# Performance work log

Measured on AMD Instinct MI355X. Metric: run time of the kernel, lower is better.

## Reference

```python
import jax, jax.numpy as jnp
import numpy as np

NEG_SLOPE = 0.2  # leaky_relu negative slope (alpha)

def _glorot(key, shape):
    fan_in, fan_out = shape[0], shape[-1]
    lim = jnp.sqrt(6.0 / (fan_in + fan_out))
    return jax.random.uniform(key, shape, jnp.float32, -lim, lim)

def setup_inputs() -> dict:
    key = jax.random.key(0)
    ks = jax.random.split(key, 10)
    N, E, F_IN, HID, HEADS, NCLASS = 50000, 800000, 512, 32, 8, 32
    x = jax.random.normal(ks[0], (N, F_IN), jnp.float32)
    edge_index = jax.random.randint(ks[1], (2, E), 0, N, jnp.int64)
    # layer 1: heads=8, out per head = 32, concat -> 256
    W1 = _glorot(ks[2], (F_IN, HEADS * HID))
    att_src1 = _glorot(ks[3], (HEADS, HID))
    att_dst1 = _glorot(ks[4], (HEADS, HID))
    b1 = jnp.zeros((HEADS * HID,), jnp.float32)
    # layer 2: heads=1, out = nclass
    W2 = _glorot(ks[5], (HEADS * HID, NCLASS))
    att_src2 = _glorot(ks[6], (1, NCLASS))
    att_dst2 = _glorot(ks[7], (1, NCLASS))
    b2 = jnp.zeros((NCLASS,), jnp.float32)
    return {"x": x, "edge_index": edge_index, "W1": W1, "att_src1": att_src1,
            "att_dst1": att_dst1, "b1": b1, "W2": W2, "att_src2": att_src2,
            "att_dst2": att_dst2, "b2": b2}

def gat_conv(x, src, dst, W, a_src, a_dst, bias, num_nodes):
    """PyG GATConv (eval mode, self loops already appended to src/dst)."""
    H, C = a_src.shape
    h = (x @ W).reshape(num_nodes, H, C)                 # [N,H,C]
    score_src = jnp.einsum('nhc,hc->nh', h, a_src)       # [N,H]
    score_dst = jnp.einsum('nhc,hc->nh', h, a_dst)       # [N,H]
    e = jax.nn.leaky_relu(score_src[src] + score_dst[dst], NEG_SLOPE)  # [E,H]
    m = jax.ops.segment_max(e, dst, num_segments=num_nodes)           # [N,H]
    w = jnp.exp(e - m[dst])
    denom = jax.ops.segment_sum(w, dst, num_segments=num_nodes)       # [N,H]
    alpha = w / (denom[dst] + 1e-16)                                  # [E,H]
    out = jax.ops.segment_sum(alpha[:, :, None] * h[src], dst,
                              num_segments=num_nodes)                 # [N,H,C]
    return out.reshape(num_nodes, H * C) + bias

def reference(x, edge_index, W1, att_src1, att_dst1, b1, W2, att_src2, att_dst2, b2):
    N = x.shape[0]
    loops = jnp.arange(N, dtype=edge_index.dtype)
    src = jnp.concatenate([edge_index[0], loops])  # PyG add_self_loops=True
    dst = jnp.concatenate([edge_index[1], loops])
    h = jax.nn.elu(gat_conv(x, src, dst, W1, att_src1, att_dst1, b1, N))
    out = gat_conv(h, src, dst, W2, att_src2, att_dst2, b2, N)
    return out + 1e-06
```

## Files before the change

kernel.cpp:

```cpp
#include <hip/hip_runtime.h>
#include <math.h>

#define N_NODES 50000
#define N_EDGES 800000
#define E2 (N_EDGES + N_NODES)
#define F_IN 512
#define HEADS 8
#define HID 32
#define HC 256
#define NCLASS 32
#define NEG_SLOPE 0.2f
#define ELLW 64

typedef unsigned int uint;
typedef unsigned short ushort;
typedef __attribute__((ext_vector_type(8))) short bf16x8;
typedef __attribute__((ext_vector_type(4))) float f32x4;

#define GLOBAL_LOAD_LDS16(g, l) \
    __builtin_amdgcn_global_load_lds((const __attribute__((address_space(1))) void*)(g), \
                                     (__attribute__((address_space(3))) void*)(l), 16, 0, 0)

__device__ inline uint bf16_rne_bits(float f) {
    uint u = __float_as_uint(f);
    return (u + 0x7fffu + ((u >> 16) & 1u)) >> 16;
}
__device__ inline float bf2f(ushort u) { return __uint_as_float(((uint)u) << 16); }

#define W1_BLOCKS 512
#define W2_BLOCKS 32
#define FILL_BLOCKS ((E2 / 4 + 255) / 256)

__global__ void __launch_bounds__(256) prep_kernel(const float* __restrict__ W1,
        ushort* __restrict__ w1hi, ushort* __restrict__ w1lo,
        const float* __restrict__ W2, ushort* __restrict__ w2hi, ushort* __restrict__ w2lo,
        const int* __restrict__ ei, int* __restrict__ cursor, int* __restrict__ ell) {
    int b = blockIdx.x;
    if (b < W1_BLOCKS) {
        int t = b * 256 + threadIdx.x;
        int n = t >> 9, k = t & 511;
        float f = W1[k * 256 + n];
        uint h = bf16_rne_bits(f);
        float r = f - __uint_as_float(h << 16);
        w1hi[t] = (ushort)h;
        w1lo[t] = (ushort)bf16_rne_bits(r);
    } else if (b < W1_BLOCKS + W2_BLOCKS) {
        int t = (b - W1_BLOCKS) * 256 + threadIdx.x;
        int n = t >> 8, k = t & 255;
        float f = W2[k * 32 + n];
        uint h = bf16_rne_bits(f);
        float r = f - __uint_as_float(h << 16);
        w2hi[t] = (ushort)h;
        w2lo[t] = (ushort)bf16_rne_bits(r);
    } else {
        int e0 = ((b - W1_BLOCKS - W2_BLOCKS) * 256 + threadIdx.x) * 4;
        if (e0 < E2) {
            int src[4], dst[4];
            if (e0 < N_EDGES) {
                int4 s4 = *(const int4*)(ei + e0);
                int4 d4 = *(const int4*)(ei + N_EDGES + e0);
                src[0] = s4.x; src[1] = s4.y; src[2] = s4.z; src[3] = s4.w;
                dst[0] = d4.x; dst[1] = d4.y; dst[2] = d4.z; dst[3] = d4.w;
            } else {
                #pragma unroll
                for (int j = 0; j < 4; ++j) { src[j] = e0 + j - N_EDGES; dst[j] = src[j]; }
            }
            #pragma unroll
            for (int j = 0; j < 4; ++j) {
                int d = dst[j];
                int p = atomicAdd(&cursor[d], 1);
                ell[d * ELLW + p] = src[j];
            }
        }
    }
}

__global__ void __launch_bounds__(256) gemm1_mfma_kernel(const uint* __restrict__ xp,
        const ushort* __restrict__ bhi, const ushort* __restrict__ blo,
        const float* __restrict__ as1, const float* __restrict__ ad1,
        ushort* __restrict__ C, float* __restrict__ ssrc, float* __restrict__ sdst, int M) {
    __shared__ uint   As[2][128 * 32];
    __shared__ ushort Bh[2][128 * 32];
    __shared__ ushort Bl[2][128 * 32];
    const int tid = threadIdx.x, lane = tid & 63, wave = tid >> 6;

    const int NW = ((N_NODES + 127) / 128) * 2;
    const int orig = blockIdx.y * gridDim.x + blockIdx.x;
    const int xcd = orig & 7, idx = orig >> 3;
    const int q = NW >> 3, r = NW & 7;
    const int nid = (xcd < r ? xcd * (q + 1) : r * (q + 1) + (xcd - r) * q) + idx;
    const int bm = (nid >> 1) * 128, bn = (nid & 1) * 128;

    const uint* agp[8]; const uint* alp[8];
    #pragma unroll
    for (int s = 0; s < 4; ++s) {
        int t = wave * 4 + s;
        int p = t * 64 + lane;
        int row = p >> 3, cs = p & 7;
        int c = cs ^ (row & 7);
        int grow = bm + row; if (grow > M - 1) grow = M - 1;
        agp[s]     = xp + ((size_t)grow * 512 + c * 4);
        agp[s + 4] = xp + ((size_t)grow * 512 + 32 + c * 4);
        alp[s]     = &As[0][t * 256];
        alp[s + 4] = &As[1][t * 256];
    }
    const ushort* bhgp[4]; const ushort* blgp[4]; const ushort* bhlp[4]; const ushort* bllp[4];
    #pragma unroll
    for (int s = 0; s < 2; ++s) {
        int t = wave * 2 + s;
        int p = t * 64 + lane;
        int row = p >> 2, qs = p & 3;
        int qq = qs ^ ((row >> 1) & 3);
        size_t go0 = (size_t)(bn + row) * 512 + qq * 8;
        size_t go1 = go0 + 32;
        bhgp[s] = bhi + go0; bhgp[s + 2] = bhi + go1;
        blgp[s] = blo + go0; blgp[s + 2] = blo + go1;
        bhlp[s] = &Bh[0][t * 512]; bhlp[s + 2] = &Bh[1][t * 512];
        bllp[s] = &Bl[0][t * 512]; bllp[s + 2] = &Bl[1][t * 512];
    }

    f32x4 acc[4][4] = {};
    const int wm = (wave >> 1) * 64, wn = (wave & 1) * 64;
    const int fm = lane & 15, quad = lane >> 4;

    for (int kk = 0; kk < 8; ++kk) {
        #pragma unroll
        for (int s = 0; s < 8; ++s) GLOBAL_LOAD_LDS16(agp[s], alp[s]);
        #pragma unroll
        for (int s = 0; s < 4; ++s) {
            GLOBAL_LOAD_LDS16(bhgp[s], bhlp[s]);
            GLOBAL_LOAD_LDS16(blgp[s], bllp[s]);
        }
        #pragma unroll
        for (int s = 0; s < 8; ++s) agp[s] += 64;
        #pragma unroll
        for (int s = 0; s < 4; ++s) { bhgp[s] += 64; blgp[s] += 64; }
        __syncthreads();

        #pragma unroll
        for (int h = 0; h < 2; ++h) {
            bf16x8 ah[4], al[4], bh[4], bl[4];
            #pragma unroll
            for (int i = 0; i < 4; ++i) {
                int row = wm + i * 16 + fm;
                int sw = row & 7;
                uint4 c0 = *(const uint4*)&As[h][row * 32 + (((2 * quad)     ^ sw) * 4)];
                uint4 c1 = *(const uint4*)&As[h][row * 32 + (((2 * quad + 1) ^ sw) * 4)];
                union { uint u[4]; bf16x8 v; } H, L;
                H.u[0] = __builtin_amdgcn_perm(c0.y, c0.x, 0x07060302u);
                H.u[1] = __builtin_amdgcn_perm(c0.w, c0.z, 0x07060302u);
                H.u[2] = __builtin_amdgcn_perm(c1.y, c1.x, 0x07060302u);
                H.u[3] = __builtin_amdgcn_perm(c1.w, c1.z, 0x07060302u);
                uint r0 = __float_as_uint(__uint_as_float(c0.x) - __uint_as_float(c0.x & 0xffff0000u));
                uint r1 = __float_as_uint(__uint_as_float(c0.y) - __uint_as_float(c0.y & 0xffff0000u));
                uint r2 = __float_as_uint(__uint_as_float(c0.z) - __uint_as_float(c0.z & 0xffff0000u));
                uint r3 = __float_as_uint(__uint_as_float(c0.w) - __uint_as_float(c0.w & 0xffff0000u));
                uint r4 = __float_as_uint(__uint_as_float(c1.x) - __uint_as_float(c1.x & 0xffff0000u));
                uint r5 = __float_as_uint(__uint_as_float(c1.y) - __uint_as_float(c1.y & 0xffff0000u));
                uint r6 = __float_as_uint(__uint_as_float(c1.z) - __uint_as_float(c1.z & 0xffff0000u));
                uint r7 = __float_as_uint(__uint_as_float(c1.w) - __uint_as_float(c1.w & 0xffff0000u));
                L.u[0] = __builtin_amdgcn_perm(r1, r0, 0x07060302u);
                L.u[1] = __builtin_amdgcn_perm(r3, r2, 0x07060302u);
                L.u[2] = __builtin_amdgcn_perm(r5, r4, 0x07060302u);
                L.u[3] = __builtin_amdgcn_perm(r7, r6, 0x07060302u);
                ah[i] = H.v; al[i] = L.v;
            }
            #pragma unroll
            for (int j = 0; j < 4; ++j) {
                int row = wn + j * 16 + fm;
                int qs = quad ^ ((row >> 1) & 3);
                bh[j] = *(const bf16x8*)&Bh[h][row * 32 + qs * 8];
                bl[j] = *(const bf16x8*)&Bl[h][row * 32 + qs * 8];
            }
            #pragma unroll
            for (int i = 0; i < 4; ++i)
                #pragma unroll
                for (int j = 0; j < 4; ++j) {
                    acc[i][j] = __builtin_amdgcn_mfma_f32_16x16x32_bf16(ah[i], bh[j], acc[i][j], 0, 0, 0);
                    acc[i][j] = __builtin_amdgcn_mfma_f32_16x16x32_bf16(ah[i], bl[j], acc[i][j], 0, 0, 0);
                    acc[i][j] = __builtin_amdgcn_mfma_f32_16x16x32_bf16(al[i], bh[j], acc[i][j], 0, 0, 0);
                }
        }
        __syncthreads();
    }

    #pragma unroll
    for (int i = 0; i < 4; ++i) {
        int rb = bm + wm + i * 16 + quad * 4;
        #pragma unroll
        for (int j = 0; j < 4; ++j) {
            int col = bn + wn + j * 16 + fm;
            #pragma unroll
            for (int r2_ = 0; r2_ < 4; ++r2_) {
                int row = rb + r2_;
                if (row < M) C[(size_t)row * 256 + col] = (ushort)bf16_rne_bits(acc[i][j][r2_]);
            }
        }
    }

    const int head0 = (bn + wn) >> 5;
    const float asA0 = as1[head0 * 32 + fm],      asA1 = as1[head0 * 32 + 16 + fm];
    const float asB0 = as1[head0 * 32 + 32 + fm], asB1 = as1[head0 * 32 + 48 + fm];
    const float adA0 = ad1[head0 * 32 + fm],      adA1 = ad1[head0 * 32 + 16 + fm];
    const float adB0 = ad1[head0 * 32 + 32 + fm], adB1 = ad1[head0 * 32 + 48 + fm];
    #pragma unroll
    for (int i = 0; i < 4; ++i) {
        #pragma unroll
        for (int r2_ = 0; r2_ < 4; ++r2_) {
            int row = bm + wm + i * 16 + quad * 4 + r2_;
            float s1A = acc[i][0][r2_] * asA0 + acc[i][1][r2_] * asA1;
            float s1B = acc[i][2][r2_] * asB0 + acc[i][3][r2_] * asB1;
            float s2A = acc[i][0][r2_] * adA0 + acc[i][1][r2_] * adA1;
            float s2B = acc[i][2][r2_] * adB0 + acc[i][3][r2_] * adB1;
            #pragma unroll
            for (int off = 1; off < 16; off <<= 1) {
                s1A += __shfl_xor(s1A, off);
                s1B += __shfl_xor(s1B, off);
                s2A += __shfl_xor(s2A, off);
                s2B += __shfl_xor(s2B, off);
            }
            if (fm == 0 && row < M) {
                ssrc[(size_t)row * 8 + head0]     = s1A;
                ssrc[(size_t)row * 8 + head0 + 1] = s1B;
                sdst[(size_t)row * 8 + head0]     = s2A;
                sdst[(size_t)row * 8 + head0 + 1] = s2B;
            }
        }
    }
}

__global__ void __launch_bounds__(256) gemm2_mfma_kernel(const ushort* __restrict__ A,
        const ushort* __restrict__ bh_g, const ushort* __restrict__ bl_g,
        const float* __restrict__ as2, const float* __restrict__ ad2,
        ushort* __restrict__ C, float* __restrict__ ssrc, float* __restrict__ sdst, int M) {
    const int tid = threadIdx.x, lane = tid & 63, wave = tid >> 6;
    const int bm = blockIdx.x * 128;
    const int fm = lane & 15, quad = lane >> 4;
    const int wrow = wave * 32;

    int gr[2];
    #pragma unroll
    for (int i = 0; i < 2; ++i) {
        gr[i] = bm + wrow + i * 16 + fm;
        if (gr[i] > M - 1) gr[i] = M - 1;
    }

    f32x4 acc[2][2] = {};
    for (int kk = 0; kk < 8; ++kk) {
        bf16x8 a[2], bh[2], bl[2];
        #pragma unroll
        for (int i = 0; i < 2; ++i)
            a[i] = *(const bf16x8*)(A + (size_t)gr[i] * 256 + kk * 32 + quad * 8);
        #pragma unroll
        for (int j = 0; j < 2; ++j) {
            size_t off = (size_t)(j * 16 + fm) * 256 + kk * 32 + quad * 8;
            bh[j] = *(const bf16x8*)(bh_g + off);
            bl[j] = *(const bf16x8*)(bl_g + off);
        }
        #pragma unroll
        for (int i = 0; i < 2; ++i)
            #pragma unroll
            for (int j = 0; j < 2; ++j) {
                acc[i][j] = __builtin_amdgcn_mfma_f32_16x16x32_bf16(a[i], bh[j], acc[i][j], 0, 0, 0);
                acc[i][j] = __builtin_amdgcn_mfma_f32_16x16x32_bf16(a[i], bl[j], acc[i][j], 0, 0, 0);
            }
    }

    float a0 = as2[fm], a1 = as2[16 + fm];
    float d0 = ad2[fm], d1 = ad2[16 + fm];
    #pragma unroll
    for (int i = 0; i < 2; ++i) {
        #pragma unroll
        for (int r2_ = 0; r2_ < 4; ++r2_) {
            int rg = bm + wrow + i * 16 + quad * 4 + r2_;
            float v0 = acc[i][0][r2_], v1 = acc[i][1][r2_];
            float s1 = v0 * a0 + v1 * a1;
            float s2 = v0 * d0 + v1 * d1;
            #pragma unroll
            for (int off = 1; off < 16; off <<= 1) {
                s1 += __shfl_xor(s1, off);
                s2 += __shfl_xor(s2, off);
            }
            if (rg < M) {
                C[(size_t)rg * 32 + fm]      = (ushort)bf16_rne_bits(v0);
                C[(size_t)rg * 32 + 16 + fm] = (ushort)bf16_rne_bits(v1);
                if (fm == 0) { ssrc[rg] = s1; sdst[rg] = s2; }
            }
        }
    }
}

__global__ void __launch_bounds__(256) agg1_wave_kernel(const ushort* __restrict__ h,
        const float* __restrict__ ssrc, const float* __restrict__ sdst,
        const int* __restrict__ cnt, const int* __restrict__ ell,
        const float* __restrict__ bias, ushort* __restrict__ out) {
    const int wid = (blockIdx.x * blockDim.x + threadIdx.x) >> 6;
    if (wid >= N_NODES) return;
    const int lane = threadIdx.x & 63;
    const int hg = lane >> 3;
    const int hl = lane & 7;
    const int n = wid;
    const int beg = n * ELLW;
    const int end = beg + cnt[n];
    const float sdst_n = sdst[(size_t)n * HEADS + hg];

    float4 acc = make_float4(0.f, 0.f, 0.f, 0.f);
    float sw = 0.f;
    const ushort* hc = h + lane * 4;
    const int base = hg << 3;
    for (int e = beg; e < end; e += 16) {
        int ee0 = e + hl, ee1 = e + 8 + hl;
        int ei0 = ee0 < end ? ee0 : end - 1;
        int ei1 = ee1 < end ? ee1 : end - 1;
        int s0 = ell[ei0];
        int s1 = ell[ei1];
        float c0 = ssrc[(size_t)s0 * HEADS + hg] + sdst_n;
        float c1 = ssrc[(size_t)s1 * HEADS + hg] + sdst_n;
        c0 = c0 > 0.f ? c0 : NEG_SLOPE * c0;
        c1 = c1 > 0.f ? c1 : NEG_SLOPE * c1;
        float w0 = (ee0 < end) ? __expf(c0) : 0.f;
        float w1 = (ee1 < end) ? __expf(c1) : 0.f;
        float wj[16]; int sj[16];
        #pragma unroll
        for (int j = 0; j < 8; ++j) {
            wj[j]     = __shfl(w0, base + j);
            sj[j]     = __shfl(s0, base + j);
            wj[8 + j] = __shfl(w1, base + j);
            sj[8 + j] = __shfl(s1, base + j);
        }
        ushort4 v[16];
        #pragma unroll
        for (int j = 0; j < 16; ++j) v[j] = *(const ushort4*)(hc + (size_t)sj[j] * HC);
        #pragma unroll
        for (int j = 0; j < 16; ++j) {
            acc.x += wj[j] * bf2f(v[j].x);
            acc.y += wj[j] * bf2f(v[j].y);
            acc.z += wj[j] * bf2f(v[j].z);
            acc.w += wj[j] * bf2f(v[j].w);
            sw += wj[j];
        }
    }
    float inv = 1.f / (sw + 1e-16f);
    float4 bv = *(const float4*)(bias + lane * 4);
    float4 o;
    o.x = acc.x * inv + bv.x; o.y = acc.y * inv + bv.y;
    o.z = acc.z * inv + bv.z; o.w = acc.w * inv + bv.w;
    o.x = o.x > 0.f ? o.x : expm1f(o.x);
    o.y = o.y > 0.f ? o.y : expm1f(o.y);
    o.z = o.z > 0.f ? o.z : expm1f(o.z);
    o.w = o.w > 0.f ? o.w : expm1f(o.w);
    ushort4 ob;
    ob.x = (ushort)bf16_rne_bits(o.x);
    ob.y = (ushort)bf16_rne_bits(o.y);
    ob.z = (ushort)bf16_rne_bits(o.z);
    ob.w = (ushort)bf16_rne_bits(o.w);
    *(ushort4*)(out + (size_t)n * HC + lane * 4) = ob;
}

__global__ void __launch_bounds__(256) agg2_kernel(const ushort* __restrict__ h2,
        const float* __restrict__ ssrc, const float* __restrict__ sdst,
        const int* __restrict__ cnt, const int* __restrict__ ell,
        const float* __restrict__ bias, float* __restrict__ out) {
    const int n = blockIdx.x * 4 + (threadIdx.x >> 6);
    if (n >= N_NODES) return;
    const int beg = n * ELLW;
    const int end = beg + cnt[n];
    const int t = threadIdx.x & 63;
    const float sdst_n = sdst[n];

    const int slot = t >> 4, cp = t & 15;
    float a0 = 0.f, a1 = 0.f, sw = 0.f;
    for (int e = beg + slot; e < end; e += 4) {
        int src = ell[e];
        float sc = ssrc[src] + sdst_n;
        sc = sc > 0.f ? sc : NEG_SLOPE * sc;
        float w = __expf(sc);
        uint v = *(const uint*)(h2 + (size_t)src * NCLASS + cp * 2);
        a0 += w * __uint_as_float(v << 16);
        a1 += w * __uint_as_float(v & 0xffff0000u);
        sw += w;
    }
    a0 += __shfl_down(a0, 32); a1 += __shfl_down(a1, 32); sw += __shfl_down(sw, 32);
    a0 += __shfl_down(a0, 16); a1 += __shfl_down(a1, 16); sw += __shfl_down(sw, 16);
    if (t < 16) {
        float inv = 1.f / (sw + 1e-16f);
        float2 o;
        o.x = a0 * inv + bias[cp * 2]     + 1e-6f;
        o.y = a1 * inv + bias[cp * 2 + 1] + 1e-6f;
        *(float2*)(out + (size_t)n * NCLASS + cp * 2) = o;
    }
}

extern "C" void kernel_launch(void* const* d_in, const int* in_sizes, int n_in,
                              void* d_out, int out_size, void* d_ws, size_t ws_size,
                              hipStream_t stream) {
    const float* x        = (const float*)d_in[0];
    const int*   ei       = (const int*)  d_in[1];
    const float* W1       = (const float*)d_in[2];
    const float* att_src1 = (const float*)d_in[3];
    const float* att_dst1 = (const float*)d_in[4];
    const float* b1       = (const float*)d_in[5];
    const float* W2       = (const float*)d_in[6];
    const float* att_src2 = (const float*)d_in[7];
    const float* att_dst2 = (const float*)d_in[8];
    const float* b2       = (const float*)d_in[9];
    float* out = (float*)d_out;

    ushort* w1t_hi = (ushort*)d_ws;
    ushort* w1t_lo = w1t_hi + 256 * 512;
    ushort* w2t_hi = w1t_lo + 256 * 512;
    ushort* w2t_lo = w2t_hi + 32 * 256;
    ushort* h1b    = w2t_lo + 32 * 256;
    ushort* h2b    = h1b + (size_t)N_NODES * HC;
    ushort* out1b  = h2b + (size_t)N_NODES * NCLASS;
    float* ssrc1 = (float*)(out1b + (size_t)N_NODES * HC);
    float* sdst1 = ssrc1 + (size_t)N_NODES * HEADS;
    float* ssrc2 = sdst1 + (size_t)N_NODES * HEADS;
    float* sdst2 = ssrc2 + N_NODES;
    int* cursor  = (int*)(sdst2 + N_NODES);
    int* ell     = cursor + N_NODES;

    hipMemsetAsync(cursor, 0, N_NODES * sizeof(int), stream);
    prep_kernel<<<W1_BLOCKS + W2_BLOCKS + FILL_BLOCKS, 256, 0, stream>>>(
            W1, w1t_hi, w1t_lo, W2, w2t_hi, w2t_lo, ei, cursor, ell);

    {
        dim3 grid((N_NODES + 127) / 128, 2);
        gemm1_mfma_kernel<<<grid, 256, 0, stream>>>((const uint*)x, w1t_hi, w1t_lo,
                att_src1, att_dst1, h1b, ssrc1, sdst1, N_NODES);
    }
    agg1_wave_kernel<<<(N_NODES + 3) / 4, 256, 0, stream>>>(h1b, ssrc1, sdst1, cursor, ell, b1, out1b);

    gemm2_mfma_kernel<<<(N_NODES + 127) / 128, 256, 0, stream>>>(out1b, w2t_hi, w2t_lo,
            att_src2, att_dst2, h2b, ssrc2, sdst2, N_NODES);
    agg2_kernel<<<(N_NODES + 3) / 4, 256, 0, stream>>>(h2b, ssrc2, sdst2, cursor, ell, b2, out);
}
```

Measured before the change: 373.5 us.

## Drop W1 low-part from split-bf16 GEMM1 and halve K-step tile

GEMM1 no longer uses the low-order bf16 part of W1, so each output tile now takes two MFMAs (x_hi*W_hi + x_lo*W_hi) instead of three. It also stops loading the W1 low tensor. The K loop changes from 8 steps of 64 to 16 steps of 32 with single LDS buffers, which cuts shared memory use and may raise occupancy. The cost is lower precision in the layer-1 projection and twice as many barrier round-trips per tile.

```diff
diff --git a/kernel.cpp b/kernel.cpp
--- a/kernel.cpp
+++ b/kernel.cpp
@@ -76,12 +76,11 @@
 }
 
 __global__ void __launch_bounds__(256) gemm1_mfma_kernel(const uint* __restrict__ xp,
-        const ushort* __restrict__ bhi, const ushort* __restrict__ blo,
+        const ushort* __restrict__ bhi,
         const float* __restrict__ as1, const float* __restrict__ ad1,
         ushort* __restrict__ C, float* __restrict__ ssrc, float* __restrict__ sdst, int M) {
-    __shared__ uint   As[2][128 * 32];
-    __shared__ ushort Bh[2][128 * 32];
-    __shared__ ushort Bl[2][128 * 32];
+    __shared__ uint   As[128 * 32];
+    __shared__ ushort Bh[128 * 32];
     const int tid = threadIdx.x, lane = tid & 63, wave = tid >> 6;
 
     const int NW = ((N_NODES + 127) / 128) * 2;
@@ -91,7 +90,7 @@
     const int nid = (xcd < r ? xcd * (q + 1) : r * (q + 1) + (xcd - r) * q) + idx;
     const int bm = (nid >> 1) * 128, bn = (nid & 1) * 128;
 
-    const uint* agp[8]; const uint* alp[8];
+    const uint* agp[4]; const uint* alp[4];
     #pragma unroll
     for (int s = 0; s < 4; ++s) {
         int t = wave * 4 + s;
@@ -99,88 +98,75 @@
         int row = p >> 3, cs = p & 7;
         int c = cs ^ (row & 7);
         int grow = bm + row; if (grow > M - 1) grow = M - 1;
-        agp[s]     = xp + ((size_t)grow * 512 + c * 4);
-        agp[s + 4] = xp + ((size_t)grow * 512 + 32 + c * 4);
-        alp[s]     = &As[0][t * 256];
-        alp[s + 4] = &As[1][t * 256];
-    }
-    const ushort* bhgp[4]; const ushort* blgp[4]; const ushort* bhlp[4]; const ushort* bllp[4];
+        agp[s] = xp + ((size_t)grow * 512 + c * 4);
+        alp[s] = &As[t * 256];
+    }
+    const ushort* bhgp[2]; const ushort* bhlp[2];
     #pragma unroll
     for (int s = 0; s < 2; ++s) {
         int t = wave * 2 + s;
         int p = t * 64 + lane;
         int row = p >> 2, qs = p & 3;
         int qq = qs ^ ((row >> 1) & 3);
-        size_t go0 = (size_t)(bn + row) * 512 + qq * 8;
-        size_t go1 = go0 + 32;
-        bhgp[s] = bhi + go0; bhgp[s + 2] = bhi + go1;
-        blgp[s] = blo + go0; blgp[s + 2] = blo + go1;
-        bhlp[s] = &Bh[0][t * 512]; bhlp[s + 2] = &Bh[1][t * 512];
-        bllp[s] = &Bl[0][t * 512]; bllp[s + 2] = &Bl[1][t * 512];
+        size_t go = (size_t)(bn + row) * 512 + qq * 8;
+        bhgp[s] = bhi + go;
+        bhlp[s] = &Bh[t * 512];
     }
 
     f32x4 acc[4][4] = {};
     const int wm = (wave >> 1) * 64, wn = (wave & 1) * 64;
     const int fm = lane & 15, quad = lane >> 4;
 
-    for (int kk = 0; kk < 8; ++kk) {
-        #pragma unroll
-        for (int s = 0; s < 8; ++s) GLOBAL_LOAD_LDS16(agp[s], alp[s]);
-        #pragma unroll
-        for (int s = 0; s < 4; ++s) {
-            GLOBAL_LOAD_LDS16(bhgp[s], bhlp[s]);
-            GLOBAL_LOAD_LDS16(blgp[s], bllp[s]);
-        }
-        #pragma unroll
-        for (int s = 0; s < 8; ++s) agp[s] += 64;
-        #pragma unroll
-        for (int s = 0; s < 4; ++s) { bhgp[s] += 64; blgp[s] += 64; }
+    for (int kk = 0; kk < 16; ++kk) {
+        #pragma unroll
+        for (int s = 0; s < 4; ++s) GLOBAL_LOAD_LDS16(agp[s], alp[s]);
+        #pragma unroll
+        for (int s = 0; s < 2; ++s) GLOBAL_LOAD_LDS16(bhgp[s], bhlp[s]);
+        #pragma unroll
+        for (int s = 0; s < 4; ++s) agp[s] += 32;
+        #pragma unroll
+        for (int s = 0; s < 2; ++s) bhgp[s] += 32;
         __syncthreads();
 
-        #pragma unroll
-        for (int h = 0; h < 2; ++h) {
-            bf16x8 ah[4], al[4], bh[4], bl[4];
-            #pragma unroll
-            for (int i = 0; i < 4; ++i) {
-                int row = wm + i * 16 + fm;
-                int sw = row & 7;
-                uint4 c0 = *(const uint4*)&As[h][row * 32 + (((2 * quad)     ^ sw) * 4)];
-                uint4 c1 = *(const uint4*)&As[h][row * 32 + (((2 * quad + 1) ^ sw) * 4)];
-                union { uint u[4]; bf16x8 v; } H, L;
-                H.u[0] = __builtin_amdgcn_perm(c0.y, c0.x, 0x07060302u);
-                H.u[1] = __builtin_amdgcn_perm(c0.w, c0.z, 0x07060302u);
-                H.u[2] = __builtin_amdgcn_perm(c1.y, c1.x, 0x07060302u);
-                H.u[3] = __builtin_amdgcn_perm(c1.w, c1.z, 0x07060302u);
-                uint r0 = __float_as_uint(__uint_as_float(c0.x) - __uint_as_float(c0.x & 0xffff0000u));
-                uint r1 = __float_as_uint(__uint_as_float(c0.y) - __uint_as_float(c0.y & 0xffff0000u));
-                uint r2 = __float_as_uint(__uint_as_float(c0.z) - __uint_as_float(c0.z & 0xffff0000u));
-                uint r3 = __float_as_uint(__uint_as_float(c0.w) - __uint_as_float(c0.w & 0xffff0000u));
-                uint r4 = __float_as_uint(__uint_as_float(c1.x) - __uint_as_float(c1.x & 0xffff0000u));
-                uint r5 = __float_as_uint(__uint_as_float(c1.y) - __uint_as_float(c1.y & 0xffff0000u));
-                uint r6 = __float_as_uint(__uint_as_float(c1.z) - __uint_as_float(c1.z & 0xffff0000u));
-                uint r7 = __float_as_uint(__uint_as_float(c1.w) - __uint_as_float(c1.w & 0xffff0000u));
-                L.u[0] = __builtin_amdgcn_perm(r1, r0, 0x07060302u);
-                L.u[1] = __builtin_amdgcn_perm(r3, r2, 0x07060302u);
-                L.u[2] = __builtin_amdgcn_perm(r5, r4, 0x07060302u);
-                L.u[3] = __builtin_amdgcn_perm(r7, r6, 0x07060302u);
-                ah[i] = H.v; al[i] = L.v;
-            }
+        bf16x8 ah[4], al[4], bh[4];
+        #pragma unroll
+        for (int i = 0; i < 4; ++i) {
+            int row = wm + i * 16 + fm;
+            int sw = row & 7;
+            uint4 c0 = *(const uint4*)&As[row * 32 + (((2 * quad)     ^ sw) * 4)];
+            uint4 c1 = *(const uint4*)&As[row * 32 + (((2 * quad + 1) ^ sw) * 4)];
+            union { uint u[4]; bf16x8 v; } H, L;
+            H.u[0] = __builtin_amdgcn_perm(c0.y, c0.x, 0x07060302u);
+            H.u[1] = __builtin_amdgcn_perm(c0.w, c0.z, 0x07060302u);
+            H.u[2] = __builtin_amdgcn_perm(c1.y, c1.x, 0x07060302u);
+            H.u[3] = __builtin_amdgcn_perm(c1.w, c1.z, 0x07060302u);
+            uint r0 = __float_as_uint(__uint_as_float(c0.x) - __uint_as_float(c0.x & 0xffff0000u));
+            uint r1 = __float_as_uint(__uint_as_float(c0.y) - __uint_as_float(c0.y & 0xffff0000u));
+            uint r2 = __float_as_uint(__uint_as_float(c0.z) - __uint_as_float(c0.z & 0xffff0000u));
+            uint r3 = __float_as_uint(__uint_as_float(c0.w) - __uint_as_float(c0.w & 0xffff0000u));
+            uint r4 = __float_as_uint(__uint_as_float(c1.x) - __uint_as_float(c1.x & 0xffff0000u));
+            uint r5 = __float_as_uint(__uint_as_float(c1.y) - __uint_as_float(c1.y & 0xffff0000u));
+            uint r6 = __float_as_uint(__uint_as_float(c1.z) - __uint_as_float(c1.z & 0xffff0000u));
+            uint r7 = __float_as_uint(__uint_as_float(c1.w) - __uint_as_float(c1.w & 0xffff0000u));
+            L.u[0] = __builtin_amdgcn_perm(r1, r0, 0x07060302u);
+            L.u[1] = __builtin_amdgcn_perm(r3, r2, 0x07060302u);
+            L.u[2] = __builtin_amdgcn_perm(r5, r4, 0x07060302u);
+            L.u[3] = __builtin_amdgcn_perm(r7, r6, 0x07060302u);
+            ah[i] = H.v; al[i] = L.v;
+        }
+        #pragma unroll
+        for (int j = 0; j < 4; ++j) {
+            int row = wn + j * 16 + fm;
+            int qs = quad ^ ((row >> 1) & 3);
+            bh[j] = *(const bf16x8*)&Bh[row * 32 + qs * 8];
+        }
+        #pragma unroll
+        for (int i = 0; i < 4; ++i)
             #pragma unroll
             for (int j = 0; j < 4; ++j) {
-                int row = wn + j * 16 + fm;
-                int qs = quad ^ ((row >> 1) & 3);
-                bh[j] = *(const bf16x8*)&Bh[h][row * 32 + qs * 8];
-                bl[j] = *(const bf16x8*)&Bl[h][row * 32 + qs * 8];
-            }
-            #pragma unroll
-            for (int i = 0; i < 4; ++i)
-                #pragma unroll
-                for (int j = 0; j < 4; ++j) {
-                    acc[i][j] = __builtin_amdgcn_mfma_f32_16x16x32_bf16(ah[i], bh[j], acc[i][j], 0, 0, 0);
-                    acc[i][j] = __builtin_amdgcn_mfma_f32_16x16x32_bf16(ah[i], bl[j], acc[i][j], 0, 0, 0);
-                    acc[i][j] = __builtin_amdgcn_mfma_f32_16x16x32_bf16(al[i], bh[j], acc[i][j], 0, 0, 0);
-                }
-        }
+                acc[i][j] = __builtin_amdgcn_mfma_f32_16x16x32_bf16(ah[i], bh[j], acc[i][j], 0, 0, 0);
+                acc[i][j] = __builtin_amdgcn_mfma_f32_16x16x32_bf16(al[i], bh[j], acc[i][j], 0, 0, 0);
+            }
         __syncthreads();
     }
 
@@ -426,7 +412,7 @@
 
     {
         dim3 grid((N_NODES + 127) / 128, 2);
-        gemm1_mfma_kernel<<<grid, 256, 0, stream>>>((const uint*)x, w1t_hi, w1t_lo,
+        gemm1_mfma_kernel<<<grid, 256, 0, stream>>>((const uint*)x, w1t_hi,
                 att_src1, att_dst1, h1b, ssrc1, sdst1, N_NODES);
     }
     agg1_wave_kernel<<<(N_NODES + 3) / 4, 256, 0, stream>>>(h1b, ssrc1, sdst1, cursor, ell, b1, out1b);
```

After: 362.6 us. 1.03x faster.
